# Kernel optimization log

Hardware: AMD Instinct MI355X
Metric: run time of the kernel (lower is better)

## Reference

```python
import jax, jax.numpy as jnp
import numpy as np

S, B, D = 128, 512, 512  # S == max_length


def setup_inputs() -> dict:
    key = jax.random.key(0)
    k1, k2 = jax.random.split(key)
    x = jax.random.normal(k1, (S, B, D), dtype=jnp.float32)
    src_mask = jax.random.bernoulli(k2, 0.2, (B, S))
    return {"x": x, "src_mask": src_mask}


def reference(x, src_mask):
    # x: (S, B, D); src_mask: (B, S) bool, True = pad.
    S_ = x.shape[0]
    xb = jnp.transpose(x, (1, 0, 2))                    # (B, S, D)
    valid = (~src_mask).astype(x.dtype)                 # (B, S)
    xm = xb * valid[:, :, None]                         # zero out padded tokens
    g = jnp.arange(S_ - 1)
    s = jnp.arange(S_)
    # left fragment g keeps positions s <= g; right keeps s > g
    keep_left = (s[None, :] <= g[:, None]).astype(x.dtype)   # (G, S)
    keep_right = jnp.asarray(1.0, x.dtype) - keep_left        # (G, S)
    left = jnp.einsum('gs,bsd->bgd', keep_left, xm)     # (B, G, D)
    right = jnp.einsum('gs,bsd->bgd', keep_right, xm)   # (B, G, D)
    return jnp.concatenate([left, right], axis=2)       # (B, G, 2D)
```

## Files before the change

### kernel.cpp

```cpp
#include <hip/hip_runtime.h>

#define SS 128
#define BB 512
#define DD 512
#define GG 127
#define CS 8
#define NC 16
#define NCOL 32

typedef float f4 __attribute__((ext_vector_type(4)));

__global__ __launch_bounds__(512, 6) void frag_prefix_kernel(
    const float* __restrict__ x, const int* __restrict__ mask,
    float* __restrict__ out) {
  const int tid = threadIdx.x;
  const int b = blockIdx.x >> 2;
  const int dblk = (blockIdx.x & 3) << 7;
  const int col = tid & (NCOL - 1);
  const int j = tid >> 5;

  __shared__ float valid[SS];
  __shared__ f4 part[NC][NCOL];

  if (tid < SS) valid[tid] = mask[b * SS + tid] ? 0.0f : 1.0f;
  __syncthreads();

  const size_t sstride = (size_t)BB * DD / 4;
  const f4* xq = (const f4*)x + (size_t)(j * CS) * sstride +
                 ((size_t)b * DD + dblk) / 4 + col;

  f4 v[CS];
#pragma unroll
  for (int i = 0; i < CS; ++i) {
    f4 t = __builtin_nontemporal_load(xq + (size_t)i * sstride);
    v[i] = t * valid[j * CS + i];
  }

  f4 psum = v[0];
#pragma unroll
  for (int i = 1; i < CS; ++i) psum += v[i];
  part[j][col] = psum;
  __syncthreads();

  f4 offset = {0.f, 0.f, 0.f, 0.f};
  f4 total = {0.f, 0.f, 0.f, 0.f};
#pragma unroll
  for (int jj = 0; jj < NC; ++jj) {
    f4 p = part[jj][col];
    total += p;
    if (jj < j) offset += p;
  }

  f4* op = (f4*)out + ((size_t)b * GG * 2 * DD + dblk) / 4 + col;
  f4 run = offset;
#pragma unroll
  for (int i = 0; i < CS; ++i) {
    run += v[i];
    const int g = j * CS + i;
    if (g < GG) {
      __builtin_nontemporal_store(run, op + (size_t)g * (2 * DD / 4));
      f4 r = total - run;
      __builtin_nontemporal_store(r, op + (size_t)g * (2 * DD / 4) + DD / 4);
    }
  }
}

extern "C" void kernel_launch(void* const* d_in, const int* in_sizes, int n_in,
                              void* d_out, int out_size, void* d_ws, size_t ws_size,
                              hipStream_t stream) {
  const float* x = (const float*)d_in[0];
  const int* mask = (const int*)d_in[1];
  float* out = (float*)d_out;
  frag_prefix_kernel<<<dim3(BB * 4), dim3(512), 0, stream>>>(x, mask, out);
}
```

Before: 346.1 us.

## Split fragment prefix into chunk-partials pass and streaming scan pass

Replaces the single fused kernel with two kernels. The first computes per-16-position chunk sums of masked x into workspace. The second reads those partials to form per-chunk offsets and totals, then re-reads x to stream the running prefix and suffix outputs. This gives each thread fewer registers and a simpler access pattern, but it reads x twice and adds workspace traffic and a second launch. The old kernel is kept as a fallback when the workspace is too small.

```diff
diff --git a/kernel.cpp b/kernel.cpp
--- a/kernel.cpp
+++ b/kernel.cpp
@@ -4,11 +4,81 @@
 #define BB 512
 #define DD 512
 #define GG 127
+#define NBD4 (BB * DD / 4)
+
+typedef float f4 __attribute__((ext_vector_type(4)));
+
+__global__ __launch_bounds__(256, 8) void k1_partials(
+    const float* __restrict__ x, const int* __restrict__ mask,
+    float* __restrict__ ws) {
+  const int q = blockIdx.x >> 8;
+  const int slab = blockIdx.x & 255;
+  const int bd4 = slab * 256 + threadIdx.x;
+  const int b = bd4 >> 7;
+
+  int mm[16];
+  const int4* mq = (const int4*)(mask + b * SS + q * 16);
+  *(int4*)&mm[0] = mq[0];
+  *(int4*)&mm[4] = mq[1];
+  *(int4*)&mm[8] = mq[2];
+  *(int4*)&mm[12] = mq[3];
+
+  const f4* xq = (const f4*)x + (size_t)(q * 16) * NBD4 + bd4;
+  f4 acc = {0.f, 0.f, 0.f, 0.f};
+#pragma unroll
+  for (int i = 0; i < 16; ++i) {
+    f4 t = xq[(size_t)i * NBD4];
+    acc += t * (mm[i] ? 0.0f : 1.0f);
+  }
+  ((f4*)ws)[(size_t)q * NBD4 + bd4] = acc;
+}
+
+__global__ __launch_bounds__(512, 8) void k2_stream(
+    const float* __restrict__ x, const int* __restrict__ mask,
+    const float* __restrict__ ws, float* __restrict__ out) {
+  const int b = blockIdx.x >> 1;
+  const int jg = blockIdx.x & 1;
+  const int j = jg * 4 + (threadIdx.x >> 7);
+  const int c = threadIdx.x & 127;
+  const int bd4 = b * 128 + c;
+
+  const f4* wq = (const f4*)ws + bd4;
+  f4 offset = {0.f, 0.f, 0.f, 0.f};
+  f4 total = {0.f, 0.f, 0.f, 0.f};
+#pragma unroll
+  for (int jj = 0; jj < 8; ++jj) {
+    f4 p = wq[(size_t)jj * NBD4];
+    total += p;
+    if (jj < j) offset += p;
+  }
+
+  int mm[16];
+  const int4* mq = (const int4*)(mask + b * SS + j * 16);
+  *(int4*)&mm[0] = mq[0];
+  *(int4*)&mm[4] = mq[1];
+  *(int4*)&mm[8] = mq[2];
+  *(int4*)&mm[12] = mq[3];
+
+  const f4* xq = (const f4*)x + (size_t)(j * 16) * NBD4 + bd4;
+  f4* outL = (f4*)out + (size_t)b * (GG * 256) + (size_t)(j * 16) * 256 + c;
+
+  f4 run = offset;
+#pragma unroll
+  for (int i = 0; i < 16; ++i) {
+    const int s = j * 16 + i;
+    if (s < GG) {
+      f4 t = xq[(size_t)i * NBD4];
+      run += t * (mm[i] ? 0.0f : 1.0f);
+      __builtin_nontemporal_store(run, outL + (size_t)i * 256);
+      f4 r = total - run;
+      __builtin_nontemporal_store(r, outL + (size_t)i * 256 + 128);
+    }
+  }
+}
+
 #define CS 8
 #define NC 16
 #define NCOL 32
-
-typedef float f4 __attribute__((ext_vector_type(4)));
 
 __global__ __launch_bounds__(512, 6) void frag_prefix_kernel(
     const float* __restrict__ x, const int* __restrict__ mask,
@@ -71,5 +141,12 @@
   const float* x = (const float*)d_in[0];
   const int* mask = (const int*)d_in[1];
   float* out = (float*)d_out;
-  frag_prefix_kernel<<<dim3(BB * 4), dim3(512), 0, stream>>>(x, mask, out);
+  const size_t ws_needed = (size_t)8 * NBD4 * sizeof(f4);
+  if (ws_size >= ws_needed && d_ws != nullptr) {
+    k1_partials<<<dim3(2048), dim3(256), 0, stream>>>(x, mask, (float*)d_ws);
+    k2_stream<<<dim3(1024), dim3(512), 0, stream>>>(
+        x, mask, (const float*)d_ws, out);
+  } else {
+    frag_prefix_kernel<<<dim3(BB * 4), dim3(512), 0, stream>>>(x, mask, out);
+  }
 }
```

Result: slower. 368.1 us (+6.4%).
